# Optimization experiments

Hardware: AMD Instinct MI355X
Metric: run time of the kernel (lower is better)

## Reference

```python
import jax, jax.numpy as jnp
import numpy as np

N, IN_CH, HID, OUT = 3072, 128, 256, 32
HEADS = 12


def setup_inputs() -> dict:
    key = jax.random.key(0)
    ks = jax.random.split(key, 16)

    def glorot(k, shape):
        fan_in, fan_out = shape[0], shape[-1]
        lim = float(np.sqrt(6.0 / (fan_in + fan_out)))
        return jax.random.uniform(k, shape, jnp.float32, -lim, lim)

    return {
        "x": jax.random.normal(ks[0], (N, IN_CH), jnp.float32),
        "attn_tensor": jax.random.normal(ks[1], (HEADS, N, N), jnp.float32),
        "edge_weight": jnp.ones((1,), jnp.float32),  # unused (use_edge_weight=False)
        "batch_idx": jnp.zeros((N,), jnp.int64),      # single graph
        # Conv2d(12,1,1) == per-head scalar mix
        "agg_w": jax.random.normal(ks[2], (HEADS,), jnp.float32) * 0.1,
        "agg_b": jnp.zeros((1,), jnp.float32),
        # GCNConv weights (x @ W then propagate, + bias)
        "W1": glorot(ks[3], (IN_CH, HID)), "b1": jnp.zeros((HID,), jnp.float32),
        "W2": glorot(ks[4], (HID, HID)),   "b2": jnp.zeros((HID,), jnp.float32),
        # final MLP: Linear -> ReLU -> LayerNorm -> Linear
        "lin1_W": glorot(ks[5], (HID, HID)), "lin1_b": jnp.zeros((HID,), jnp.float32),
        "ln_g": jnp.ones((HID,), jnp.float32), "ln_b": jnp.zeros((HID,), jnp.float32),
        "lin2_W": glorot(ks[6], (HID, OUT)), "lin2_b": jnp.zeros((OUT,), jnp.float32),
    }


def reference(x, attn_tensor, edge_weight, batch_idx,
              agg_w, agg_b, W1, b1, W2, b2,
              lin1_W, lin1_b, ln_g, ln_b, lin2_W, lin2_b):
    threshold = 0.0
    n = x.shape[0]

    # Conv2d(12,1,kernel_size=1): weighted sum over heads -> [N, N] score matrix
    agg = jnp.einsum('c,cij->ij', agg_w, attn_tensor) + agg_b[0]

    # thresholded adjacency (mask.nonzero() -> edge_index), kept dense in jax
    A = (agg > threshold).astype(x.dtype)  # A[s, t] = edge s->t

    # PyG gcn_norm with add_remaining_self_loops (binary weights -> diag = 1)
    eye = jnp.eye(n, dtype=x.dtype)
    A_hat = A * (1.0 - eye) + eye
    deg = A_hat.sum(axis=0)                        # in-degree at target nodes
    dinv = jnp.where(deg > 0, jax.lax.rsqrt(deg), 0.0)
    A_norm = dinv[:, None] * A_hat * dinv[None, :]  # norm = dinv[src] * dinv[dst]

    # GCNConv 1: out[t] = sum_s A_norm[s,t] (x W)[s] + b
    h = jnp.einsum('st,sd->td', A_norm, x @ W1) + b1
    h = jax.nn.relu(h)
    # GCNConv 2
    h = jnp.einsum('st,sd->td', A_norm, h @ W2) + b2

    # global_mean_pool over batch_idx (single graph here)
    bi = batch_idx.astype(jnp.int32)
    sums = jax.ops.segment_sum(h, bi, num_segments=1)
    counts = jax.ops.segment_sum(jnp.ones((n,), h.dtype), bi, num_segments=1)
    g = sums / counts[:, None]

    # Linear -> ReLU -> LayerNorm -> Linear
    z = jax.nn.relu(g @ lin1_W + lin1_b)
    mu = z.mean(axis=-1, keepdims=True)
    var = ((z - mu) ** 2).mean(axis=-1, keepdims=True)
    z = (z - mu) * jax.lax.rsqrt(var + 1e-5) * ln_g + ln_b
    out = z @ lin2_W + lin2_b
    return out
```

## Files before the change

### kernel.cpp

```cpp
#include <hip/hip_runtime.h>
#include <hip/hip_bf16.h>

#define NN     3072
#define NW32   96
#define NB8    384
#define INCH   128
#define HID    256
#define NHEADS 12
#define PLANE  9437184LL

typedef __attribute__((ext_vector_type(8))) short     s16x8;
typedef __attribute__((ext_vector_type(4))) float     f32x4;
typedef __attribute__((ext_vector_type(8))) unsigned short u16x8;
typedef __attribute__((ext_vector_type(4))) unsigned int   u32x4;

__device__ inline unsigned short bf16_rne(float f) {
    unsigned int u = __float_as_uint(f);
    u += 0x7FFFu + ((u >> 16) & 1u);
    return (unsigned short)(u >> 16);
}

__global__ __launch_bounds__(256) void k_adj_y1(const float* __restrict__ attn,
                                                const float* __restrict__ agg_w,
                                                const float* __restrict__ agg_b,
                                                const float* __restrict__ x,
                                                const float* __restrict__ W1,
                                                unsigned char* __restrict__ maskT8,
                                                unsigned short* __restrict__ y1t) {
    __shared__ unsigned char lb[4][1024];
    __shared__ float xs[8][INCH];

    if (blockIdx.x < 1152) {
        const int w = threadIdx.x >> 6, l = threadIdx.x & 63;
        const int t0 = (blockIdx.x % 3) * 1024;
        const int s0 = (blockIdx.x / 3) * 8;
        const int r0 = s0 + 2 * w;
        const float thr = -agg_b[0];

        f32x4 acc[2][4];
#pragma unroll
        for (int r = 0; r < 2; ++r)
#pragma unroll
            for (int q = 0; q < 4; ++q) acc[r][q] = (f32x4){0.f, 0.f, 0.f, 0.f};

        const float* base0 = attn + (long long)r0 * NN + t0 + 4 * l;
#pragma unroll 1
        for (int c = 0; c < NHEADS; ++c) {
            const float wcv = agg_w[c];
            const float* pc = base0 + (long long)c * PLANE;
#pragma unroll
            for (int r = 0; r < 2; ++r) {
#pragma unroll
                for (int q = 0; q < 4; ++q) {
                    f32x4 v = *(const f32x4*)(pc + r * NN + q * 256);
                    acc[r][q][0] = fmaf(wcv, v[0], acc[r][q][0]);
                    acc[r][q][1] = fmaf(wcv, v[1], acc[r][q][1]);
                    acc[r][q][2] = fmaf(wcv, v[2], acc[r][q][2]);
                    acc[r][q][3] = fmaf(wcv, v[3], acc[r][q][3]);
                }
            }
        }

#pragma unroll
        for (int q = 0; q < 4; ++q) {
#pragma unroll
            for (int j = 0; j < 4; ++j) {
                const int tt = q * 256 + 4 * l + j;
                const int t  = t0 + tt;
                unsigned b0 = (acc[0][q][j] > thr || r0 == t)     ? 1u : 0u;
                unsigned b1 = (acc[1][q][j] > thr || r0 + 1 == t) ? 1u : 0u;
                lb[w][tt] = (unsigned char)(b0 | (b1 << 1));
            }
        }
        __syncthreads();
        const int sb = s0 >> 3;
        for (int k = threadIdx.x; k < 1024; k += 256) {
            unsigned v = (unsigned)lb[0][k] | ((unsigned)lb[1][k] << 2)
                       | ((unsigned)lb[2][k] << 4) | ((unsigned)lb[3][k] << 6);
            maskT8[(long long)(t0 + k) * NB8 + sb] = (unsigned char)v;
        }
    } else {
        int s0 = (blockIdx.x - 1152) * 8;
        for (int i = threadIdx.x; i < 8 * INCH; i += 256)
            xs[i >> 7][i & 127] = x[s0 * INCH + i];
        __syncthreads();
        int d = threadIdx.x;
        float acc[8] = {0, 0, 0, 0, 0, 0, 0, 0};
        for (int k = 0; k < INCH; ++k) {
            float w = W1[k * HID + d];
#pragma unroll
            for (int r = 0; r < 8; ++r) acc[r] = fmaf(xs[r][k], w, acc[r]);
        }
        u16x8 v;
#pragma unroll
        for (int r = 0; r < 8; ++r) v[r] = bf16_rne(acc[r]);
        *(u16x8*)(y1t + (long long)d * NN + s0) = v;
    }
}

__global__ __launch_bounds__(256) void k_dinv(const unsigned int* __restrict__ maskT32,
                                              float* __restrict__ dinv,
                                              unsigned short* __restrict__ dinvb) {
    int t = blockIdx.x * 256 + threadIdx.x;
    const u32x4* row = (const u32x4*)(maskT32 + (long long)t * NW32);
    int deg = 0;
#pragma unroll
    for (int i = 0; i < 24; ++i) {
        u32x4 v = row[i];
        deg += __popc(v[0]) + __popc(v[1]) + __popc(v[2]) + __popc(v[3]);
    }
    float di = rsqrtf((float)deg);
    dinv[t] = di;
    dinvb[t] = bf16_rne(di);
}

__global__ __launch_bounds__(256) void k_prop(const unsigned int* __restrict__ maskT32,
                                              const unsigned short* __restrict__ dinvb,
                                              const unsigned short* __restrict__ y1t,
                                              const float* __restrict__ dinv,
                                              float* __restrict__ partials,
                                              float* __restrict__ w2p) {
    if (blockIdx.x < 384) {
        const int w = threadIdx.x >> 6, l = threadIdx.x & 63;
        const int lr = l & 15, lg = l >> 4;
        const int t0 = (blockIdx.x % 48) * 64 + w * 16;
        const int d0 = ((blockIdx.x / 48) % 2) * 128;
        const int z  = blockIdx.x / 96;

        const unsigned long long* mrow =
            (const unsigned long long*)(maskT32 + (long long)(t0 + lr) * NW32) + z * 12;

        const unsigned short* B[8];
#pragma unroll
        for (int n = 0; n < 8; ++n)
            B[n] = y1t + (long long)(d0 + n * 16 + lr) * NN;

        f32x4 acc[8];
#pragma unroll
        for (int n = 0; n < 8; ++n) acc[n] = (f32x4){0.f, 0.f, 0.f, 0.f};

#pragma unroll 2
        for (int kw = 0; kw < 12; ++kw) {
            unsigned long long word = mrow[kw];
#pragma unroll
            for (int half = 0; half < 2; ++half) {
                const int k0 = z * 768 + kw * 64 + half * 32 + lg * 8;
                unsigned int bits = (unsigned int)((word >> (half * 32 + lg * 8)) & 0xFFULL);
                u16x8 dv = *(const u16x8*)(dinvb + k0);
                s16x8 av;
#pragma unroll
                for (int j = 0; j < 8; ++j)
                    av[j] = ((bits >> j) & 1u) ? (short)dv[j] : (short)0;
#pragma unroll
                for (int n = 0; n < 8; ++n) {
                    s16x8 bv = *(const s16x8*)(const void*)(B[n] + k0);
                    acc[n] = __builtin_amdgcn_mfma_f32_16x16x32_bf16(av, bv, acc[n], 0, 0, 0);
                }
            }
        }

        const int trow = t0 + lg * 4;
#pragma unroll
        for (int n = 0; n < 8; ++n) {
            const int d = d0 + n * 16 + lr;
#pragma unroll
            for (int r = 0; r < 4; ++r)
                partials[((size_t)z * NN + trow + r) * HID + d] = acc[n][r];
        }
    } else {
        __shared__ float red[4][64];
        const int r = blockIdx.x - 384;
        const int wq = r % 48;
        const int tc = r / 48;
        const int wv = threadIdx.x >> 6, l = threadIdx.x & 63;
        const unsigned long long* mt = (const unsigned long long*)maskT32;
        float acc = 0.0f;
#pragma unroll 4
        for (int it = 0; it < 64; ++it) {
            const int t = tc * 256 + wv * 64 + it;
            unsigned long long word = mt[(long long)t * 48 + wq];
            acc += ((word >> l) & 1ULL) ? dinv[t] : 0.0f;
        }
        red[wv][l] = acc;
        __syncthreads();
        if (threadIdx.x < 64)
            w2p[tc * NN + wq * 64 + threadIdx.x] =
                red[0][threadIdx.x] + red[1][threadIdx.x] + red[2][threadIdx.x] + red[3][threadIdx.x];
    }
}

__global__ __launch_bounds__(256) void k_vred(const float* __restrict__ partials,
                                              const float* __restrict__ dinv,
                                              const float* __restrict__ b1,
                                              const float* __restrict__ w2p,
                                              float* __restrict__ vp) {
    __shared__ float w2s[8];
    const int b = blockIdx.x, d = threadIdx.x;
    if (threadIdx.x < 8) {
        const int t = b * 8 + threadIdx.x;
        float a = 0.0f;
#pragma unroll
        for (int tc = 0; tc < 12; ++tc) a += w2p[tc * NN + t];
        w2s[threadIdx.x] = dinv[t] * a;
    }
    __syncthreads();
    const float bb = b1[d];
    float vacc = 0.0f;
#pragma unroll
    for (int i = 0; i < 8; ++i) {
        const int t = b * 8 + i;
        float ssum = partials[((size_t)0 * NN + t) * HID + d]
                   + partials[((size_t)1 * NN + t) * HID + d]
                   + partials[((size_t)2 * NN + t) * HID + d]
                   + partials[((size_t)3 * NN + t) * HID + d];
        float h = fmaxf(fmaf(dinv[t], ssum, bb), 0.0f);
        vacc = fmaf(w2s[i], h, vacc);
    }
    vp[b * HID + d] = vacc;
}

__global__ __launch_bounds__(256) void k_head(const float* __restrict__ vp,
                                              const float* __restrict__ W2,
                                              const float* __restrict__ b2,
                                              const float* __restrict__ l1W,
                                              const float* __restrict__ l1b,
                                              const float* __restrict__ lng,
                                              const float* __restrict__ lnb,
                                              const float* __restrict__ l2W,
                                              const float* __restrict__ l2b,
                                              float* __restrict__ out) {
    __shared__ float vs[HID], gs[HID], zs[HID], red[4];
    int d = threadIdx.x;
    float v = 0.0f;
    for (int c = 0; c < 384; ++c) v += vp[c * HID + d];
    vs[d] = v;
    __syncthreads();
    float a = 0.0f;
    for (int k = 0; k < HID; ++k) a = fmaf(vs[k], W2[k * HID + d], a);
    gs[d] = b2[d] + a * (1.0f / 3072.0f);
    __syncthreads();
    float z1 = l1b[d];
    for (int k = 0; k < HID; ++k) z1 = fmaf(gs[k], l1W[k * HID + d], z1);
    z1 = fmaxf(z1, 0.0f);
    float sum = z1;
    for (int o = 1; o < 64; o <<= 1) sum += __shfl_xor(sum, o);
    if ((d & 63) == 0) red[d >> 6] = sum;
    __syncthreads();
    float mu = (red[0] + red[1] + red[2] + red[3]) * (1.0f / 256.0f);
    __syncthreads();
    float diff = z1 - mu, sq = diff * diff;
    for (int o = 1; o < 64; o <<= 1) sq += __shfl_xor(sq, o);
    if ((d & 63) == 0) red[d >> 6] = sq;
    __syncthreads();
    float var = (red[0] + red[1] + red[2] + red[3]) * (1.0f / 256.0f);
    float zn = diff * rsqrtf(var + 1e-5f) * lng[d] + lnb[d];
    zs[d] = zn;
    __syncthreads();
    if (d < 32) {
        float o = l2b[d];
        for (int k = 0; k < HID; ++k) o = fmaf(zs[k], l2W[k * 32 + d], o);
        out[d] = o;
    }
}

extern "C" void kernel_launch(void* const* d_in, const int* in_sizes, int n_in,
                              void* d_out, int out_size, void* d_ws, size_t ws_size,
                              hipStream_t stream) {
    const float* x     = (const float*)d_in[0];
    const float* attn  = (const float*)d_in[1];
    const float* agg_w = (const float*)d_in[4];
    const float* agg_b = (const float*)d_in[5];
    const float* W1    = (const float*)d_in[6];
    const float* b1    = (const float*)d_in[7];
    const float* W2    = (const float*)d_in[8];
    const float* b2    = (const float*)d_in[9];
    const float* l1W   = (const float*)d_in[10];
    const float* l1b   = (const float*)d_in[11];
    const float* lng   = (const float*)d_in[12];
    const float* lnb   = (const float*)d_in[13];
    const float* l2W   = (const float*)d_in[14];
    const float* l2b   = (const float*)d_in[15];
    float* out = (float*)d_out;

    char* ws = (char*)d_ws;
    size_t off = 0;
    auto alloc = [&](size_t bytes) -> void* {
        off = (off + 255) & ~(size_t)255;
        void* p = ws + off;
        off += bytes;
        return p;
    };
    unsigned int*   maskT32 = (unsigned int*)alloc((size_t)NN * NW32 * 4);
    float*          dinv  = (float*)alloc((size_t)NN * 4);
    unsigned short* dinvb = (unsigned short*)alloc((size_t)NN * 2);
    float*          w2p   = (float*)alloc((size_t)12 * NN * 4);
    unsigned short* y1t   = (unsigned short*)alloc((size_t)HID * NN * 2);
    float*          part  = (float*)alloc((size_t)4 * NN * HID * 4);
    float*          vp    = (float*)alloc((size_t)384 * HID * 4);

    hipLaunchKernelGGL(k_adj_y1, dim3(1536), dim3(256), 0, stream,
                       attn, agg_w, agg_b, x, W1, (unsigned char*)maskT32, y1t);
    hipLaunchKernelGGL(k_dinv,   dim3(12),   dim3(256), 0, stream, maskT32, dinv, dinvb);
    hipLaunchKernelGGL(k_prop,   dim3(960),  dim3(256), 0, stream,
                       maskT32, dinvb, y1t, dinv, part, w2p);
    hipLaunchKernelGGL(k_vred,   dim3(384),  dim3(256), 0, stream, part, dinv, b1, w2p, vp);
    hipLaunchKernelGGL(k_head,   dim3(1),    dim3(256), 0, stream,
                       vp, W2, b2, l1W, l1b, lng, lnb, l2W, l2b, out);
}
```

Before: 193.3 us.

## Stream attention planes contiguously into row-major bitmask, then transpose with ballot kernel

The adjacency kernel now has each block read contiguous 2048-float pieces of each head plane, with 6 slabs per block. It packs the thresholded bits into a row-major 32-bit mask through a shared nibble buffer, where the old version scattered transposed byte writes. A new k_pack kernel transposes 64x64 bit tiles with wave ballots to produce the transposed mask that later stages consume. The aim is fully coalesced streaming of the 450MB attention tensor and no scattered byte stores. The cost is an extra launch, extra mask traffic and a modulo test for the diagonal.

```diff
diff --git a/kernel.cpp b/kernel.cpp
--- a/kernel.cpp
+++ b/kernel.cpp
@@ -3,11 +3,14 @@
 
 #define NN     3072
 #define NW32   96
-#define NB8    384
 #define INCH   128
 #define HID    256
 #define NHEADS 12
 #define PLANE  9437184LL
+#define PIECEF 2048
+#define NADJ   768
+#define SLABF  (NADJ*PIECEF)
+#define NSLAB  6
 
 typedef __attribute__((ext_vector_type(8))) short     s16x8;
 typedef __attribute__((ext_vector_type(4))) float     f32x4;
@@ -25,62 +28,64 @@
                                                 const float* __restrict__ agg_b,
                                                 const float* __restrict__ x,
                                                 const float* __restrict__ W1,
-                                                unsigned char* __restrict__ maskT8,
+                                                unsigned int* __restrict__ mask32,
                                                 unsigned short* __restrict__ y1t) {
-    __shared__ unsigned char lb[4][1024];
+    __shared__ unsigned char nib[512];
     __shared__ float xs[8][INCH];
 
-    if (blockIdx.x < 1152) {
-        const int w = threadIdx.x >> 6, l = threadIdx.x & 63;
-        const int t0 = (blockIdx.x % 3) * 1024;
-        const int s0 = (blockIdx.x / 3) * 8;
-        const int r0 = s0 + 2 * w;
+    if (blockIdx.x < NADJ) {
+        const int b = blockIdx.x;
+        const int j = threadIdx.x;
         const float thr = -agg_b[0];
-
-        f32x4 acc[2][4];
-#pragma unroll
-        for (int r = 0; r < 2; ++r)
-#pragma unroll
-            for (int q = 0; q < 4; ++q) acc[r][q] = (f32x4){0.f, 0.f, 0.f, 0.f};
-
-        const float* base0 = attn + (long long)r0 * NN + t0 + 4 * l;
+        float wc[NHEADS];
+#pragma unroll
+        for (int c = 0; c < NHEADS; ++c) wc[c] = agg_w[c];
+
 #pragma unroll 1
-        for (int c = 0; c < NHEADS; ++c) {
-            const float wcv = agg_w[c];
-            const float* pc = base0 + (long long)c * PLANE;
-#pragma unroll
-            for (int r = 0; r < 2; ++r) {
-#pragma unroll
-                for (int q = 0; q < 4; ++q) {
-                    f32x4 v = *(const f32x4*)(pc + r * NN + q * 256);
-                    acc[r][q][0] = fmaf(wcv, v[0], acc[r][q][0]);
-                    acc[r][q][1] = fmaf(wcv, v[1], acc[r][q][1]);
-                    acc[r][q][2] = fmaf(wcv, v[2], acc[r][q][2]);
-                    acc[r][q][3] = fmaf(wcv, v[3], acc[r][q][3]);
+        for (int i = 0; i < NSLAB; ++i) {
+            const int P = i * SLABF + b * PIECEF;
+
+            f32x4 acc[2];
+            acc[0] = (f32x4){0.f, 0.f, 0.f, 0.f};
+            acc[1] = (f32x4){0.f, 0.f, 0.f, 0.f};
+#pragma unroll 1
+            for (int c = 0; c < NHEADS; ++c) {
+                const float* pc = attn + (long long)c * PLANE + P;
+                f32x4 v0 = *(const f32x4*)(pc + 4 * j);
+                f32x4 v1 = *(const f32x4*)(pc + 4 * (256 + j));
+                const float w = wc[c];
+#pragma unroll
+                for (int k = 0; k < 4; ++k) {
+                    acc[0][k] = fmaf(w, v0[k], acc[0][k]);
+                    acc[1][k] = fmaf(w, v1[k], acc[1][k]);
                 }
             }
-        }
-
-#pragma unroll
-        for (int q = 0; q < 4; ++q) {
-#pragma unroll
-            for (int j = 0; j < 4; ++j) {
-                const int tt = q * 256 + 4 * l + j;
-                const int t  = t0 + tt;
-                unsigned b0 = (acc[0][q][j] > thr || r0 == t)     ? 1u : 0u;
-                unsigned b1 = (acc[1][q][j] > thr || r0 + 1 == t) ? 1u : 0u;
-                lb[w][tt] = (unsigned char)(b0 | (b1 << 1));
+
+#pragma unroll
+            for (int q = 0; q < 2; ++q) {
+                const int g = q * 256 + j;
+                const unsigned off0 = (unsigned)P + 4u * g;
+                unsigned bits = 0;
+#pragma unroll
+                for (int k = 0; k < 4; ++k) {
+                    const unsigned off = off0 + k;
+                    bool pred = (acc[q][k] > thr) || (off % 3073u == 0u);
+                    bits |= pred ? (1u << k) : 0u;
+                }
+                nib[g] = (unsigned char)bits;
             }
-        }
-        __syncthreads();
-        const int sb = s0 >> 3;
-        for (int k = threadIdx.x; k < 1024; k += 256) {
-            unsigned v = (unsigned)lb[0][k] | ((unsigned)lb[1][k] << 2)
-                       | ((unsigned)lb[2][k] << 4) | ((unsigned)lb[3][k] << 6);
-            maskT8[(long long)(t0 + k) * NB8 + sb] = (unsigned char)v;
+            __syncthreads();
+            if (j < 64) {
+                unsigned a = *(const unsigned*)(nib + 8 * j);
+                unsigned c2 = *(const unsigned*)(nib + 8 * j + 4);
+                a &= 0x0F0F0F0Fu;  a = (a | (a >> 4)) & 0x00FF00FFu;  a = (a | (a >> 8)) & 0x0000FFFFu;
+                c2 &= 0x0F0F0F0Fu; c2 = (c2 | (c2 >> 4)) & 0x00FF00FFu; c2 = (c2 | (c2 >> 8)) & 0x0000FFFFu;
+                mask32[(P >> 5) + j] = a | (c2 << 16);
+            }
+            __syncthreads();
         }
     } else {
-        int s0 = (blockIdx.x - 1152) * 8;
+        int s0 = (blockIdx.x - NADJ) * 8;
         for (int i = threadIdx.x; i < 8 * INCH; i += 256)
             xs[i >> 7][i & 127] = x[s0 * INCH + i];
         __syncthreads();
@@ -95,6 +100,21 @@
 #pragma unroll
         for (int r = 0; r < 8; ++r) v[r] = bf16_rne(acc[r]);
         *(u16x8*)(y1t + (long long)d * NN + s0) = v;
+    }
+}
+
+__global__ __launch_bounds__(256) void k_pack(const unsigned int* __restrict__ mask32,
+                                              unsigned long long* __restrict__ maskT64) {
+    const int w = threadIdx.x >> 6, l = threadIdx.x & 63;
+    const int tile = blockIdx.x * 4 + w;
+    const int sq = tile % 48, tq = tile / 48;
+    const unsigned long long* m64 = (const unsigned long long*)mask32;
+    unsigned long long myw = m64[(long long)(sq * 64 + l) * 48 + tq];
+#pragma unroll 8
+    for (int tt = 0; tt < 64; ++tt) {
+        unsigned long long bal = __ballot((myw >> tt) & 1ULL);
+        if (l == tt)
+            maskT64[(long long)(tq * 64 + tt) * 48 + sq] = bal;
     }
 }
 
@@ -290,6 +310,7 @@
         off += bytes;
         return p;
     };
+    unsigned int*   mask32  = (unsigned int*)alloc((size_t)NN * NW32 * 4);
     unsigned int*   maskT32 = (unsigned int*)alloc((size_t)NN * NW32 * 4);
     float*          dinv  = (float*)alloc((size_t)NN * 4);
     unsigned short* dinvb = (unsigned short*)alloc((size_t)NN * 2);
@@ -298,8 +319,10 @@
     float*          part  = (float*)alloc((size_t)4 * NN * HID * 4);
     float*          vp    = (float*)alloc((size_t)384 * HID * 4);
 
-    hipLaunchKernelGGL(k_adj_y1, dim3(1536), dim3(256), 0, stream,
-                       attn, agg_w, agg_b, x, W1, (unsigned char*)maskT32, y1t);
+    hipLaunchKernelGGL(k_adj_y1, dim3(1152), dim3(256), 0, stream,
+                       attn, agg_w, agg_b, x, W1, mask32, y1t);
+    hipLaunchKernelGGL(k_pack,   dim3(576),  dim3(256), 0, stream,
+                       mask32, (unsigned long long*)maskT32);
     hipLaunchKernelGGL(k_dinv,   dim3(12),   dim3(256), 0, stream, maskT32, dinv, dinvb);
     hipLaunchKernelGGL(k_prop,   dim3(960),  dim3(256), 0, stream,
                        maskT32, dinvb, y1t, dinv, part, w2p);
```

New measurement: 186.6 us. 1.04x faster.
